# Kernel tuning notes

Hardware: AMD Instinct MI355X
Metric: run time of the kernel (lower is better)

The kernel has to match this reference:

```python
import jax, jax.numpy as jnp
import numpy as np

IN_C, OUT_C, K, N_FILTERS, STRIDE, PAD = 256, 512, 3, 64, 1, 1


def setup_inputs() -> dict:
    key = jax.random.key(0)
    kx, kw, kb, krw, krb = jax.random.split(key, 5)
    fan_in = IN_C * K * K
    bound = 1.0 / np.sqrt(fan_in)
    x = jax.random.normal(kx, (32, IN_C, 56, 56), dtype=jnp.float32)
    weight = jax.random.uniform(kw, (OUT_C, IN_C, K, K), minval=-bound, maxval=bound, dtype=jnp.float32)
    bias = jax.random.uniform(kb, (OUT_C,), minval=-bound, maxval=bound, dtype=jnp.float32)
    rbound = 1.0 / np.sqrt(IN_C)
    router_w = jax.random.uniform(krw, (OUT_C, IN_C), minval=-rbound, maxval=rbound, dtype=jnp.float32)
    router_b = jax.random.uniform(krb, (OUT_C,), minval=-rbound, maxval=rbound, dtype=jnp.float32)
    return {"x": x, "weight": weight, "bias": bias, "router_w": router_w, "router_b": router_b}


def reference(x, weight, bias, router_w, router_b):
    B = x.shape[0]
    # router: global avg pool -> linear -> top-k channel mask
    pooled = jnp.mean(x, axis=(2, 3))                      # [B, IN_C]
    router_out = pooled @ router_w.T + router_b            # [B, OUT_C]
    _, top_idx = jax.lax.top_k(router_out, N_FILTERS)      # [B, k]
    mask = jnp.zeros((B, OUT_C), dtype=x.dtype).at[jnp.arange(B)[:, None], top_idx].set(1.0)
    # dense conv2d
    conv = jax.lax.conv_general_dilated(
        x, weight, window_strides=(STRIDE, STRIDE), padding=[(PAD, PAD), (PAD, PAD)],
        dimension_numbers=("NCHW", "OIHW", "NCHW"))
    conv = conv + bias[None, :, None, None]
    return conv * mask[:, :, None, None]
```

## Files before the change

### kernel.cpp

```cpp
#include <hip/hip_runtime.h>

#define IN_C   256
#define OUT_C  512
#define WIDTH  56
#define HW     3136
#define KTOT   2304
#define NF     64
#define NU     448
#define NB     32
#define NGRP   8
#define TN     128
#define NTILE  25
#define XROWS  242
#define LDX    40

typedef __bf16 bf16x8 __attribute__((ext_vector_type(8)));
typedef float  f32x4  __attribute__((ext_vector_type(4)));

__global__ __launch_bounds__(256) void pool_kernel(const float* __restrict__ x,
                                                   float* __restrict__ pooled) {
    int bc = blockIdx.x;
    const float* src = x + (size_t)bc * HW;
    float s = 0.f;
    for (int i = threadIdx.x; i < HW; i += 256) s += src[i];
    #pragma unroll
    for (int off = 32; off > 0; off >>= 1) s += __shfl_down(s, off, 64);
    __shared__ float wsum[4];
    int lane = threadIdx.x & 63, wv = threadIdx.x >> 6;
    if (lane == 0) wsum[wv] = s;
    __syncthreads();
    if (threadIdx.x == 0)
        pooled[bc] = (wsum[0] + wsum[1] + wsum[2] + wsum[3]) * (1.0f / HW);
}

__global__ __launch_bounds__(512) void router_kernel(const float* __restrict__ pooled,
                                                     const float* __restrict__ rw,
                                                     const float* __restrict__ rb,
                                                     int* __restrict__ sel,
                                                     int* __restrict__ unsel) {
    int b = blockIdx.x;
    __shared__ float p[IN_C];
    __shared__ float v[OUT_C];
    __shared__ int   scount, ucount;
    int t = threadIdx.x;
    if (t < IN_C) p[t] = pooled[b * IN_C + t];
    if (t == 0) { scount = 0; ucount = 0; }
    __syncthreads();
    float acc = rb[t];
    const float* wrow = rw + (size_t)t * IN_C;
    for (int i = 0; i < IN_C; ++i) acc += p[i] * wrow[i];
    v[t] = acc;
    __syncthreads();
    int cnt = 0;
    for (int j = 0; j < OUT_C; ++j) {
        float o = v[j];
        cnt += (o > acc) || (o == acc && j < t);
    }
    if (cnt < NF) {
        int pos = atomicAdd(&scount, 1);
        sel[b * NF + pos] = t;
    } else {
        int pos = atomicAdd(&ucount, 1);
        unsel[b * NU + pos] = t;
    }
}

__global__ __launch_bounds__(256) void compact_w(const float* __restrict__ w,
                                                 const int* __restrict__ sel,
                                                 __bf16* __restrict__ Acomp) {
    int id = blockIdx.x;
    int b = id / 72, rem = id - b * 72;
    int g = rem / 9, tap = rem - g * 9;
    int t = threadIdx.x;
    int oc = t >> 2, q = t & 3;
    int s = sel[b * NF + oc];
    const float* wsrc = w + (size_t)s * KTOT + tap;
    bf16x8 o;
    #pragma unroll
    for (int j = 0; j < 8; ++j)
        o[j] = (__bf16)wsrc[(g * 32 + q * 8 + j) * 9];
    *(bf16x8*)&Acomp[((size_t)id * 64 + oc) * 32 + q * 8] = o;
}

__global__ __launch_bounds__(256, 4) void conv_kernel(const float* __restrict__ x,
                                                      const __bf16* __restrict__ Acomp,
                                                      const float* __restrict__ bias,
                                                      const int* __restrict__ sel,
                                                      const int* __restrict__ unsel,
                                                      float* __restrict__ out) {
    int id   = blockIdx.x;
    int xcd  = id & 7, slot = id >> 3;
    int bq   = slot / NTILE;
    int tile = slot - bq * NTILE;
    int b    = xcd * 4 + bq;
    int ptile = tile * TN;

    int t    = threadIdx.x;
    int lane = t & 63, wv = t >> 6;
    int fm   = lane & 15, fq = lane >> 4;
    int n_base = wv * 32;

    __shared__ __bf16 xlds[2][XROWS * LDX];

    const float*  x_b    = x + (size_t)b * IN_C * HW;
    const __bf16* a_base = Acomp + (size_t)b * (NGRP * 9 * 64 * 32);

    int pp[2], poh[2], pow_[2];
    #pragma unroll
    for (int s = 0; s < 2; ++s) {
        int p = ptile + n_base + s * 16 + fm;
        pp[s] = p;
        int pc = p < HW ? p : HW - 1;
        poh[s]  = pc / WIDTH;
        pow_[s] = pc - poh[s] * WIDTH;
    }

    int  sp   = t;
    bool sact = sp < XROWS;
    int  gp   = ptile - 57 + sp;
    gp = gp < 0 ? 0 : (gp > HW - 1 ? HW - 1 : gp);
    const float* sx = x_b + gp;

    if (sact) {
        #pragma unroll
        for (int oct = 0; oct < 4; ++oct) {
            float v[8];
            #pragma unroll
            for (int j = 0; j < 8; ++j) v[j] = sx[(size_t)(oct * 8 + j) * HW];
            bf16x8 o;
            #pragma unroll
            for (int j = 0; j < 8; ++j) o[j] = (__bf16)v[j];
            *(bf16x8*)&xlds[0][sp * LDX + oct * 8] = o;
        }
    }
    __syncthreads();

    f32x4 acc[4][2] = {};
    float pre[32];

    for (int g = 0; g < NGRP; ++g) {
        int cur = g & 1;
        if (g < NGRP - 1 && sact) {
            #pragma unroll
            for (int i = 0; i < 32; ++i)
                pre[i] = sx[(size_t)((g + 1) * 32 + i) * HW];
        }
        const __bf16* gp_a = a_base + (size_t)g * 9 * 64 * 32;
        #pragma unroll
        for (int t9 = 0; t9 < 9; ++t9) {
            const int r = t9 / 3, c = t9 - 3 * (t9 / 3);
            const int shift = (r - 1) * WIDTH + (c - 1);
            const __bf16* ap = gp_a + (size_t)t9 * 64 * 32;
            bf16x8 af[4];
            #pragma unroll
            for (int mi = 0; mi < 4; ++mi)
                af[mi] = *(const bf16x8*)(ap + (size_t)(mi * 16 + fm) * 32 + fq * 8);
            #pragma unroll
            for (int s = 0; s < 2; ++s) {
                int ohr = poh[s] + r - 1, owc = pow_[s] + c - 1;
                bool ok = ((unsigned)ohr < 56u) && ((unsigned)owc < 56u);
                int n = n_base + s * 16 + fm;
                bf16x8 bfr = *(const bf16x8*)&xlds[cur][(n + 57 + shift) * LDX + fq * 8];
                bf16x8 z = {};
                bfr = ok ? bfr : z;
                #pragma unroll
                for (int mi = 0; mi < 4; ++mi)
                    acc[mi][s] = __builtin_amdgcn_mfma_f32_16x16x32_bf16(af[mi], bfr, acc[mi][s], 0, 0, 0);
            }
        }
        if (g < NGRP - 1) {
            if (sact) {
                #pragma unroll
                for (int oct = 0; oct < 4; ++oct) {
                    bf16x8 o;
                    #pragma unroll
                    for (int j = 0; j < 8; ++j) o[j] = (__bf16)pre[oct * 8 + j];
                    *(bf16x8*)&xlds[cur ^ 1][sp * LDX + oct * 8] = o;
                }
            }
            __syncthreads();
        }
    }

    const int* selb = sel + b * NF;
    size_t outb = (size_t)b * OUT_C * HW;
    #pragma unroll
    for (int mi = 0; mi < 4; ++mi) {
        #pragma unroll
        for (int reg = 0; reg < 4; ++reg) {
            int m  = mi * 16 + fq * 4 + reg;
            int oc = selb[m];
            float bs = bias[oc];
            float* orow = out + outb + (size_t)oc * HW;
            #pragma unroll
            for (int s = 0; s < 2; ++s)
                if (pp[s] < HW) orow[pp[s]] = acc[mi][s][reg] + bs;
        }
    }

    {
        const int* unselb = unsel + b * NU;
        int j = t & 31;
        bool jok = (ptile + j * 4) < HW;
        float4 z = {0.f, 0.f, 0.f, 0.f};
        for (int u = t >> 5; u < NU; u += 8) {
            int oc = unselb[u];
            if (jok)
                *(float4*)(out + outb + (size_t)oc * HW + ptile + j * 4) = z;
        }
    }
}

extern "C" void kernel_launch(void* const* d_in, const int* in_sizes, int n_in,
                              void* d_out, int out_size, void* d_ws, size_t ws_size,
                              hipStream_t stream) {
    (void)in_sizes; (void)n_in; (void)ws_size; (void)out_size;
    const float* x        = (const float*)d_in[0];
    const float* weight   = (const float*)d_in[1];
    const float* bias     = (const float*)d_in[2];
    const float* router_w = (const float*)d_in[3];
    const float* router_b = (const float*)d_in[4];
    float* out = (float*)d_out;

    char* ws = (char*)d_ws;
    float*  pooled = (float*)ws;
    int*    sel    = (int*)(ws + 32768);
    int*    unsel  = (int*)(ws + 40960);
    __bf16* Acomp  = (__bf16*)(ws + 131072);

    pool_kernel<<<NB * IN_C, 256, 0, stream>>>(x, pooled);
    router_kernel<<<NB, OUT_C, 0, stream>>>(pooled, router_w, router_b, sel, unsel);
    compact_w<<<NB * NGRP * 9, 256, 0, stream>>>(weight, sel, Acomp);

    conv_kernel<<<NTILE * NB, 256, 0, stream>>>(x, Acomp, bias, sel, unsel, out);
}
```

Before: 406.3 us.

## Convert full weight once, gather selected rows in conv, interleave zero-fill

compact_w now converts the full 512-channel weight to bf16 once per launch, with no per-batch gather, and runs before the router. The conv kernel indexes the selected rows through per-lane sel values. The zero-fill of unselected channels is spread across the channel-group loop with nontemporal stores, so it can overlap the compute and the x staging loads. Other changes: x prefetch loads moved after the MFMA section, the padding mask precomputed as bitmasks with a zero LDS row replacing the select, the pool kernel vectorised to float4, and the occupancy hint removed from launch bounds. The cost is a larger weight buffer, scattered A-fragment loads, and higher register pressure.

```diff
diff --git a/kernel.cpp b/kernel.cpp
--- a/kernel.cpp
+++ b/kernel.cpp
@@ -13,16 +13,21 @@
 #define NTILE  25
 #define XROWS  242
 #define LDX    40
+#define SLAB   (XROWS * LDX)
 
 typedef __bf16 bf16x8 __attribute__((ext_vector_type(8)));
 typedef float  f32x4  __attribute__((ext_vector_type(4)));
+typedef float  f32x2  __attribute__((ext_vector_type(2)));
 
 __global__ __launch_bounds__(256) void pool_kernel(const float* __restrict__ x,
                                                    float* __restrict__ pooled) {
     int bc = blockIdx.x;
-    const float* src = x + (size_t)bc * HW;
+    const float4* src = (const float4*)(x + (size_t)bc * HW);
     float s = 0.f;
-    for (int i = threadIdx.x; i < HW; i += 256) s += src[i];
+    for (int i = threadIdx.x; i < HW / 4; i += 256) {
+        float4 v = src[i];
+        s += v.x + v.y + v.z + v.w;
+    }
     #pragma unroll
     for (int off = 32; off > 0; off >>= 1) s += __shfl_down(s, off, 64);
     __shared__ float wsum[4];
@@ -66,28 +71,29 @@
 }
 
 __global__ __launch_bounds__(256) void compact_w(const float* __restrict__ w,
-                                                 const int* __restrict__ sel,
                                                  __bf16* __restrict__ Acomp) {
-    int id = blockIdx.x;
-    int b = id / 72, rem = id - b * 72;
-    int g = rem / 9, tap = rem - g * 9;
+    int gt = blockIdx.x;
+    int g = gt / 9, tap = gt - g * 9;
     int t = threadIdx.x;
-    int oc = t >> 2, q = t & 3;
-    int s = sel[b * NF + oc];
-    const float* wsrc = w + (size_t)s * KTOT + tap;
-    bf16x8 o;
-    #pragma unroll
-    for (int j = 0; j < 8; ++j)
-        o[j] = (__bf16)wsrc[(g * 32 + q * 8 + j) * 9];
-    *(bf16x8*)&Acomp[((size_t)id * 64 + oc) * 32 + q * 8] = o;
-}
-
-__global__ __launch_bounds__(256, 4) void conv_kernel(const float* __restrict__ x,
-                                                      const __bf16* __restrict__ Acomp,
-                                                      const float* __restrict__ bias,
-                                                      const int* __restrict__ sel,
-                                                      const int* __restrict__ unsel,
-                                                      float* __restrict__ out) {
+    #pragma unroll
+    for (int i = 0; i < 8; ++i) {
+        int idx = i * 256 + t;
+        int oc = idx >> 2, q = idx & 3;
+        const float* wsrc = w + (size_t)oc * KTOT + tap;
+        bf16x8 o;
+        #pragma unroll
+        for (int j = 0; j < 8; ++j)
+            o[j] = (__bf16)wsrc[(g * 32 + q * 8 + j) * 9];
+        *(bf16x8*)&Acomp[((size_t)gt * 512 + oc) * 32 + q * 8] = o;
+    }
+}
+
+__global__ __launch_bounds__(256) void conv_kernel(const float* __restrict__ x,
+                                                   const __bf16* __restrict__ Acomp,
+                                                   const float* __restrict__ bias,
+                                                   const int* __restrict__ sel,
+                                                   const int* __restrict__ unsel,
+                                                   float* __restrict__ out) {
     int id   = blockIdx.x;
     int xcd  = id & 7, slot = id >> 3;
     int bq   = slot / NTILE;
@@ -98,29 +104,43 @@
     int t    = threadIdx.x;
     int lane = t & 63, wv = t >> 6;
     int fm   = lane & 15, fq = lane >> 4;
-    int n_base = wv * 32;
-
-    __shared__ __bf16 xlds[2][XROWS * LDX];
-
-    const float*  x_b    = x + (size_t)b * IN_C * HW;
-    const __bf16* a_base = Acomp + (size_t)b * (NGRP * 9 * 64 * 32);
-
-    int pp[2], poh[2], pow_[2];
+
+    __shared__ __bf16 xlds[2 * SLAB + 32];
+
+    size_t outb = (size_t)b * OUT_C * HW;
+    const float* x_b = x + (size_t)b * IN_C * HW;
+
+    const int* selb = sel + b * NF;
+    int selv[4];
+    #pragma unroll
+    for (int mi = 0; mi < 4; ++mi) selv[mi] = selb[mi * 16 + fm];
+
+    const int* ub_all = unsel + b * NU + wv * 112;
+    int oc_a = ub_all[lane & 63];
+    int oc_b = (lane < 48) ? ub_all[64 + lane] : 0;
+
+    int pp[2]; unsigned okb[2] = {0u, 0u};
     #pragma unroll
     for (int s = 0; s < 2; ++s) {
-        int p = ptile + n_base + s * 16 + fm;
+        int p = ptile + wv * 32 + s * 16 + fm;
         pp[s] = p;
         int pc = p < HW ? p : HW - 1;
-        poh[s]  = pc / WIDTH;
-        pow_[s] = pc - poh[s] * WIDTH;
-    }
-
-    int  sp   = t;
-    bool sact = sp < XROWS;
-    int  gp   = ptile - 57 + sp;
+        int poh = pc / WIDTH, pow_ = pc - (pc / WIDTH) * WIDTH;
+        #pragma unroll
+        for (int t9 = 0; t9 < 9; ++t9) {
+            int r = t9 / 3, c = t9 - 3 * (t9 / 3);
+            unsigned ok = ((unsigned)(poh + r - 1) < 56u) && ((unsigned)(pow_ + c - 1) < 56u);
+            okb[s] |= ok << t9;
+        }
+    }
+
+    int  srow = wv * 61 + lane;
+    bool sact = (lane < 61) && (srow < XROWS);
+    int  gp   = ptile - 57 + srow;
     gp = gp < 0 ? 0 : (gp > HW - 1 ? HW - 1 : gp);
     const float* sx = x_b + gp;
 
+    if (t < 32) xlds[2 * SLAB + t] = (__bf16)0.f;
     if (sact) {
         #pragma unroll
         for (int oct = 0; oct < 4; ++oct) {
@@ -130,83 +150,97 @@
             bf16x8 o;
             #pragma unroll
             for (int j = 0; j < 8; ++j) o[j] = (__bf16)v[j];
-            *(bf16x8*)&xlds[0][sp * LDX + oct * 8] = o;
+            *(bf16x8*)&xlds[srow * LDX + oct * 8] = o;
         }
     }
     __syncthreads();
 
     f32x4 acc[4][2] = {};
-    float pre[32];
-
+    const int zidx = 2 * SLAB + fq * 8;
+    int pxb = ptile + lane * 2;
+    bool pok = pxb < HW;
+
+    #pragma unroll 1
     for (int g = 0; g < NGRP; ++g) {
-        int cur = g & 1;
-        if (g < NGRP - 1 && sact) {
-            #pragma unroll
-            for (int i = 0; i < 32; ++i)
-                pre[i] = sx[(size_t)((g + 1) * 32 + i) * HW];
-        }
-        const __bf16* gp_a = a_base + (size_t)g * 9 * 64 * 32;
+        int bufc = (g & 1) * SLAB;
+        int baseS[2];
+        #pragma unroll
+        for (int s = 0; s < 2; ++s)
+            baseS[s] = bufc + (57 + wv * 32 + s * 16 + fm) * LDX + fq * 8;
+
+        const __bf16* agt = Acomp + (size_t)(g * 9) * 512 * 32;
         #pragma unroll
         for (int t9 = 0; t9 < 9; ++t9) {
             const int r = t9 / 3, c = t9 - 3 * (t9 / 3);
-            const int shift = (r - 1) * WIDTH + (c - 1);
-            const __bf16* ap = gp_a + (size_t)t9 * 64 * 32;
+            const int shiftC = ((r - 1) * WIDTH + (c - 1)) * LDX;
+            const __bf16* ap = agt + (size_t)t9 * 512 * 32;
             bf16x8 af[4];
             #pragma unroll
             for (int mi = 0; mi < 4; ++mi)
-                af[mi] = *(const bf16x8*)(ap + (size_t)(mi * 16 + fm) * 32 + fq * 8);
+                af[mi] = *(const bf16x8*)(ap + (size_t)selv[mi] * 32 + fq * 8);
             #pragma unroll
             for (int s = 0; s < 2; ++s) {
-                int ohr = poh[s] + r - 1, owc = pow_[s] + c - 1;
-                bool ok = ((unsigned)ohr < 56u) && ((unsigned)owc < 56u);
-                int n = n_base + s * 16 + fm;
-                bf16x8 bfr = *(const bf16x8*)&xlds[cur][(n + 57 + shift) * LDX + fq * 8];
-                bf16x8 z = {};
-                bfr = ok ? bfr : z;
+                int idx = ((okb[s] >> t9) & 1u) ? (baseS[s] + shiftC) : zidx;
+                bf16x8 bfr = *(const bf16x8*)&xlds[idx];
                 #pragma unroll
                 for (int mi = 0; mi < 4; ++mi)
                     acc[mi][s] = __builtin_amdgcn_mfma_f32_16x16x32_bf16(af[mi], bfr, acc[mi][s], 0, 0, 0);
             }
         }
+
         if (g < NGRP - 1) {
+            float v[32];
             if (sact) {
+                const float* sx2 = sx + (size_t)((g + 1) * 32) * HW;
+                #pragma unroll
+                for (int i = 0; i < 32; ++i) v[i] = sx2[(size_t)i * HW];
+            }
+            #pragma unroll
+            for (int i = 0; i < 14; ++i) {
+                int j  = g * 14 + i;
+                int oc = (j < 64) ? __builtin_amdgcn_readlane(oc_a, j)
+                                  : __builtin_amdgcn_readlane(oc_b, j - 64);
+                if (pok) {
+                    f32x2 z2 = {0.f, 0.f};
+                    __builtin_nontemporal_store(z2, (f32x2*)(out + outb + (size_t)oc * HW + pxb));
+                }
+            }
+            if (sact) {
+                int dst = (SLAB - bufc) + srow * LDX;
                 #pragma unroll
                 for (int oct = 0; oct < 4; ++oct) {
                     bf16x8 o;
                     #pragma unroll
-                    for (int j = 0; j < 8; ++j) o[j] = (__bf16)pre[oct * 8 + j];
-                    *(bf16x8*)&xlds[cur ^ 1][sp * LDX + oct * 8] = o;
+                    for (int j = 0; j < 8; ++j) o[j] = (__bf16)v[oct * 8 + j];
+                    *(bf16x8*)&xlds[dst + oct * 8] = o;
                 }
             }
             __syncthreads();
-        }
-    }
-
-    const int* selb = sel + b * NF;
-    size_t outb = (size_t)b * OUT_C * HW;
+        } else {
+            #pragma unroll
+            for (int i = 0; i < 14; ++i) {
+                int j  = g * 14 + i;
+                int oc = (j < 64) ? __builtin_amdgcn_readlane(oc_a, j)
+                                  : __builtin_amdgcn_readlane(oc_b, j - 64);
+                if (pok) {
+                    f32x2 z2 = {0.f, 0.f};
+                    __builtin_nontemporal_store(z2, (f32x2*)(out + outb + (size_t)oc * HW + pxb));
+                }
+            }
+        }
+    }
+
     #pragma unroll
     for (int mi = 0; mi < 4; ++mi) {
         #pragma unroll
         for (int reg = 0; reg < 4; ++reg) {
-            int m  = mi * 16 + fq * 4 + reg;
-            int oc = selb[m];
+            int oc = selb[mi * 16 + fq * 4 + reg];
             float bs = bias[oc];
             float* orow = out + outb + (size_t)oc * HW;
             #pragma unroll
             for (int s = 0; s < 2; ++s)
-                if (pp[s] < HW) orow[pp[s]] = acc[mi][s][reg] + bs;
-        }
-    }
-
-    {
-        const int* unselb = unsel + b * NU;
-        int j = t & 31;
-        bool jok = (ptile + j * 4) < HW;
-        float4 z = {0.f, 0.f, 0.f, 0.f};
-        for (int u = t >> 5; u < NU; u += 8) {
-            int oc = unselb[u];
-            if (jok)
-                *(float4*)(out + outb + (size_t)oc * HW + ptile + j * 4) = z;
+                if (pp[s] < HW)
+                    __builtin_nontemporal_store(acc[mi][s][reg] + bs, &orow[pp[s]]);
         }
     }
 }
@@ -228,9 +262,9 @@
     int*    unsel  = (int*)(ws + 40960);
     __bf16* Acomp  = (__bf16*)(ws + 131072);
 
+    compact_w<<<NGRP * 9, 256, 0, stream>>>(weight, Acomp);
     pool_kernel<<<NB * IN_C, 256, 0, stream>>>(x, pooled);
     router_kernel<<<NB, OUT_C, 0, stream>>>(pooled, router_w, router_b, sel, unsel);
-    compact_w<<<NB * NGRP * 9, 256, 0, stream>>>(weight, sel, Acomp);
 
     conv_kernel<<<NTILE * NB, 256, 0, stream>>>(x, Acomp, bias, sel, unsel, out);
 }
```

Measured after the change: 417.8 us. +2.8%, slower.
